# Kernel optimization log

Hardware: AMD Instinct MI355X
Metric: run time of the kernel (lower is better)

The kernel has to match this reference:

```python
import jax, jax.numpy as jnp
import numpy as np

FACTOR = 3.0        # second_match_factor
MAX_DIST = 20.0     # second_match_max_dist
MATCHED_2 = 2       # SPIKE_MATCHED_2
CLID_UNMATCHED = 0

N, S, K = 1_000_000, 64, 32


def setup_inputs() -> dict:
    key = jax.random.key(0)
    k1, k2 = jax.random.split(key)
    return {
        "spikes": jax.random.normal(k1, (N, S), dtype=jnp.float32),
        "sort_idx": jax.random.randint(k2, (N,), 0, K, dtype=jnp.int32),
        "match_idx": jnp.zeros((N,), dtype=jnp.int32),
        "distance": jnp.zeros((N,), dtype=jnp.float32),
        "num_clusters": K,
    }


def reference(spikes, sort_idx, match_idx, distance, num_clusters):
    # spikes: (N, S) float32; sort_idx/match_idx: (N,) int; distance: (N,) float32
    n, s = spikes.shape
    k = int(num_clusters)

    # --- get_means: per-cluster mean waveform and scalar std (sqrt of summed per-dim variance)
    ones = jnp.ones((n,), spikes.dtype)
    counts = jax.ops.segment_sum(ones, sort_idx, num_segments=k)            # (K,)
    sums = jax.ops.segment_sum(spikes, sort_idx, num_segments=k)            # (K, S)
    sumsq = jax.ops.segment_sum(spikes * spikes, sort_idx, num_segments=k)  # (K, S)
    safe = jnp.maximum(counts, 1.0)[:, None]
    means = sums / safe                                                     # (K, S) templates
    var = sumsq / safe - means * means                                      # biased var (np.var ddof=0)
    stds = jnp.sqrt(jnp.maximum(var.sum(axis=1), 0.0))                      # (K,)
    valid = (jnp.arange(k) != CLID_UNMATCHED) & (counts > 0)                # exclude unmatched/empty

    x2 = (spikes * spikes).sum(axis=1, keepdims=True)                       # (N, 1)
    t2 = (means * means).sum(axis=1)                                        # (K,)
    d2 = x2 - 2.0 * (spikes @ means.T) + t2[None, :]
    dist = jnp.sqrt(jnp.maximum(d2, 1e-12))                                 # (N, K)

    # --- threshold mask (> factor*std -> inf) fused with invalid-cluster mask, then argmin
    inf = jnp.asarray(jnp.inf, dist.dtype)
    masked = jnp.where((dist > FACTOR * stds[None, :]) | ~valid[None, :], inf, dist)
    minima = masked.min(axis=1)                                             # (N,)
    minimizers = masked.argmin(axis=1).astype(sort_idx.dtype)               # cluster ids == segment ids
    minimizers = jnp.where(minima >= MAX_DIST * s, CLID_UNMATCHED, minimizers)

    # --- write back only for previously-unmatched spikes (the torch loop covers exactly these)
    unmatched = sort_idx == CLID_UNMATCHED
    new_sort = jnp.where(unmatched, minimizers, sort_idx)
    new_match = jnp.where(unmatched, MATCHED_2, match_idx)
    new_dist = jnp.where(unmatched, minima, distance)
    return new_sort, new_match, new_dist
```

## Files before the change

kernel.cpp:

```cpp
#include <hip/hip_runtime.h>
#include <math.h>

#define SDIM 64
#define KCL  32
#define NPART (KCL*SDIM*2 + KCL)
#define FACTOR_D 3.0
#define MAXDIST_TH 1280.0
#define MATCHED2_F 2.0f

#define SB 1024
#define ST 512
#define BATCH 128

#define ACHUNK 512

__global__ __launch_bounds__(ST) void stats_kernel(
    const float* __restrict__ spikes, const int* __restrict__ sortidx,
    float* __restrict__ pws, int n)
{
  __shared__ float rows[BATCH * SDIM];
  const int lane  = threadIdx.x & 63;
  const int w     = threadIdx.x >> 6;
  const int cbase = w * 4;

  float s0=0,s1=0,s2=0,s3=0;
  float q0=0,q1=0,q2=0,q3=0;
  float cn0=0,cn1=0,cn2=0,cn3=0;

  const long long nbatch = ((long long)n + BATCH - 1) / BATCH;
  const size_t gmax = (size_t)n * SDIM * sizeof(float) - 16;

  float4 v0, v1, v2, v3;
  int ida, idb;

#define LOADBATCH(B)                                                         \
  {                                                                          \
    const long long bsafe = ((B) < nbatch) ? (B) : 0;                        \
    size_t g0 = (size_t)bsafe * BATCH * SDIM * sizeof(float) +               \
                (size_t)threadIdx.x * 16;                                    \
    size_t g1 = g0 + 8192, g2 = g0 + 16384, g3 = g0 + 24576;                 \
    if (g0 > gmax) g0 = gmax;                                                \
    if (g1 > gmax) g1 = gmax;                                                \
    if (g2 > gmax) g2 = gmax;                                                \
    if (g3 > gmax) g3 = gmax;                                                \
    v0 = *reinterpret_cast<const float4*>((const char*)spikes + g0);         \
    v1 = *reinterpret_cast<const float4*>((const char*)spikes + g1);         \
    v2 = *reinterpret_cast<const float4*>((const char*)spikes + g2);         \
    v3 = *reinterpret_cast<const float4*>((const char*)spikes + g3);         \
    const long long ra = bsafe * BATCH + lane, rb = ra + 64;                 \
    ida = ((B) < nbatch && ra < n) ? sortidx[ra] : -1;                       \
    idb = ((B) < nbatch && rb < n) ? sortidx[rb] : -1;                       \
  }

#define POPLOOP(m0,m1,m2,m3,BASE)                                            \
  while (m0 | m1 | m2 | m3) {                                                \
    const bool e0 = m0 != 0, e1 = m1 != 0, e2 = m2 != 0, e3 = m3 != 0;       \
    const int b0 = e0 ? __ffsll(m0) - 1 : 0;                                 \
    const int b1 = e1 ? __ffsll(m1) - 1 : 0;                                 \
    const int b2 = e2 ? __ffsll(m2) - 1 : 0;                                 \
    const int b3 = e3 ? __ffsll(m3) - 1 : 0;                                 \
    m0 &= m0 - 1; m1 &= m1 - 1; m2 &= m2 - 1; m3 &= m3 - 1;                  \
    const float x0 = rows[((BASE) + b0) * SDIM + lane];                      \
    const float x1 = rows[((BASE) + b1) * SDIM + lane];                      \
    const float x2 = rows[((BASE) + b2) * SDIM + lane];                      \
    const float x3 = rows[((BASE) + b3) * SDIM + lane];                      \
    const float y0 = e0 ? x0 : 0.0f, y1 = e1 ? x1 : 0.0f;                    \
    const float y2 = e2 ? x2 : 0.0f, y3 = e3 ? x3 : 0.0f;                    \
    s0 += y0; q0 = fmaf(y0, x0, q0); cn0 += e0 ? 1.0f : 0.0f;                \
    s1 += y1; q1 = fmaf(y1, x1, q1); cn1 += e1 ? 1.0f : 0.0f;                \
    s2 += y2; q2 = fmaf(y2, x2, q2); cn2 += e2 ? 1.0f : 0.0f;                \
    s3 += y3; q3 = fmaf(y3, x3, q3); cn3 += e3 ? 1.0f : 0.0f;                \
  }

  long long bi = blockIdx.x;
  LOADBATCH(bi);

  for (; bi < nbatch; bi += gridDim.x) {
    __syncthreads();
    {
      char* lb = (char*)rows + (size_t)threadIdx.x * 16;
      *reinterpret_cast<float4*>(lb)         = v0;
      *reinterpret_cast<float4*>(lb + 8192)  = v1;
      *reinterpret_cast<float4*>(lb + 16384) = v2;
      *reinterpret_cast<float4*>(lb + 24576) = v3;
    }
    const int cA = ida, cB = idb;
    __syncthreads();

    LOADBATCH(bi + gridDim.x);

    unsigned long long mA0 = __ballot(cA == cbase + 0);
    unsigned long long mA1 = __ballot(cA == cbase + 1);
    unsigned long long mA2 = __ballot(cA == cbase + 2);
    unsigned long long mA3 = __ballot(cA == cbase + 3);
    unsigned long long mB0 = __ballot(cB == cbase + 0);
    unsigned long long mB1 = __ballot(cB == cbase + 1);
    unsigned long long mB2 = __ballot(cB == cbase + 2);
    unsigned long long mB3 = __ballot(cB == cbase + 3);
    if (w == 0) { mA0 = 0; mB0 = 0; }

    POPLOOP(mA0, mA1, mA2, mA3, 0)
    POPLOOP(mB0, mB1, mB2, mB3, 64)
  }
#undef LOADBATCH
#undef POPLOOP

  float* pb = pws + (size_t)blockIdx.x * NPART;
  pb[(cbase + 0) * SDIM + lane] = s0;
  pb[(cbase + 1) * SDIM + lane] = s1;
  pb[(cbase + 2) * SDIM + lane] = s2;
  pb[(cbase + 3) * SDIM + lane] = s3;
  pb[KCL * SDIM + (cbase + 0) * SDIM + lane] = q0;
  pb[KCL * SDIM + (cbase + 1) * SDIM + lane] = q1;
  pb[KCL * SDIM + (cbase + 2) * SDIM + lane] = q2;
  pb[KCL * SDIM + (cbase + 3) * SDIM + lane] = q3;
  if (lane == 0) {
    pb[2 * KCL * SDIM + cbase + 0] = cn0;
    pb[2 * KCL * SDIM + cbase + 1] = cn1;
    pb[2 * KCL * SDIM + cbase + 2] = cn2;
    pb[2 * KCL * SDIM + cbase + 3] = cn3;
  }
}

__global__ __launch_bounds__(1024) void reduce_kernel(
    const float* __restrict__ pws, double* __restrict__ gstats, int nb)
{
  __shared__ double s_acc[16][64];
  const int lane = threadIdx.x & 63;
  const int w    = threadIdx.x >> 6;
  const int u    = blockIdx.x * 64 + lane;
  double acc = 0.0;
  if (u < NPART)
    for (int b = w; b < nb; b += 16)
      acc += (double)pws[(size_t)b * NPART + u];
  s_acc[w][lane] = acc;
  __syncthreads();
  if (w == 0 && u < NPART) {
    double t = 0.0;
#pragma unroll
    for (int j = 0; j < 16; ++j) t += s_acc[j][lane];
    gstats[u] = t;
  }
}

__global__ __launch_bounds__(256) void finalize_kernel(
    const double* __restrict__ gstats, float* __restrict__ means_cs,
    double* __restrict__ t2, double* __restrict__ thr, int* __restrict__ validk)
{
  __shared__ double s_var[KCL], s_t2[KCL];
  if (threadIdx.x < KCL) { s_var[threadIdx.x] = 0.0; s_t2[threadIdx.x] = 0.0; }
  __syncthreads();
  const double* gsum = gstats;
  const double* gsq  = gstats + KCL * SDIM;
  const double* gcnt = gstats + 2 * KCL * SDIM;
  for (int i = threadIdx.x; i < KCL * SDIM; i += blockDim.x) {
    const int c = i / SDIM;
    const double cnt  = gcnt[c];
    const double safe = fmax(cnt, 1.0);
    const double m    = gsum[i] / safe;
    const double var  = gsq[i] / safe - m * m;
    means_cs[i] = (float)m;
    unsafeAtomicAdd(&s_var[c], var);
    unsafeAtomicAdd(&s_t2[c], m * m);
  }
  __syncthreads();
  if (threadIdx.x < KCL) {
    const int c = threadIdx.x;
    thr[c]    = FACTOR_D * sqrt(fmax(s_var[c], 0.0));
    t2[c]     = s_t2[c];
    validk[c] = (c != 0 && gcnt[c] > 0.0) ? 1 : 0;
  }
}

__global__ __launch_bounds__(256) void assign2_kernel(
    const float* __restrict__ spikes, const int* __restrict__ sortidx,
    const int* __restrict__ matchidx, const float* __restrict__ distance,
    const float* __restrict__ means_cs, const double* __restrict__ t2g,
    const double* __restrict__ thrg, const int* __restrict__ validk,
    float* __restrict__ out, int n)
{
  __shared__ float  s_m[KCL][SDIM];
  __shared__ double s_t2[KCL], s_thr[KCL];
  __shared__ int    s_valid[KCL];
  __shared__ int    ids[ACHUNK];
  __shared__ int    scnt;

  for (int i = threadIdx.x; i < KCL * SDIM; i += blockDim.x)
    (&s_m[0][0])[i] = means_cs[i];
  if (threadIdx.x < KCL) {
    s_t2[threadIdx.x]    = t2g[threadIdx.x];
    s_thr[threadIdx.x]   = thrg[threadIdx.x];
    s_valid[threadIdx.x] = validk[threadIdx.x];
  }
  if (threadIdx.x == 0) scnt = 0;
  __syncthreads();

  const long long start = (long long)blockIdx.x * ACHUNK;
  long long end = start + ACHUNK; if (end > n) end = n;

  for (long long i = start + threadIdx.x; i < end; i += blockDim.x) {
    const int cv = sortidx[i];
    if (cv != 0) {
      out[i]           = (float)cv;
      out[n + i]       = (float)matchidx[i];
      out[2LL * n + i] = distance[i];
    } else {
      const int p = atomicAdd(&scnt, 1);
      ids[p] = (int)i;
    }
  }
  __syncthreads();
  const int cnt = scnt;

  for (int base = 0; base < cnt; base += blockDim.x) {
    const int j = base + threadIdx.x;
    if (j >= cnt) break;
    const int r = ids[j];

    float4 xv[16];
    const float4* rp = reinterpret_cast<const float4*>(
        spikes + (size_t)r * SDIM);
#pragma unroll
    for (int s4 = 0; s4 < 16; ++s4) xv[s4] = rp[s4];

    float x2 = 0.0f;
#pragma unroll
    for (int s4 = 0; s4 < 16; ++s4) {
      x2 = fmaf(xv[s4].x, xv[s4].x, x2);
      x2 = fmaf(xv[s4].y, xv[s4].y, x2);
      x2 = fmaf(xv[s4].z, xv[s4].z, x2);
      x2 = fmaf(xv[s4].w, xv[s4].w, x2);
    }

    double best = (double)INFINITY;
    int bidx = 0;
    for (int c = 0; c < KCL; ++c) {
      float dot = 0.0f;
#pragma unroll
      for (int s4 = 0; s4 < 16; ++s4) {
        const float4 m = *reinterpret_cast<const float4*>(&s_m[c][s4 * 4]);
        dot = fmaf(xv[s4].x, m.x, dot);
        dot = fmaf(xv[s4].y, m.y, dot);
        dot = fmaf(xv[s4].z, m.z, dot);
        dot = fmaf(xv[s4].w, m.w, dot);
      }
      if (s_valid[c]) {
        const double d2 = (double)x2 - 2.0 * (double)dot + s_t2[c];
        double dist = sqrt(fmax(d2, 1e-12));
        if (dist <= s_thr[c] && dist < best) { best = dist; bidx = c; }
      }
    }

    const int mz = (best >= MAXDIST_TH) ? 0 : bidx;
    out[r]           = (float)mz;
    out[n + r]       = MATCHED2_F;
    out[2LL * n + r] = (float)best;
  }
}

extern "C" void kernel_launch(void* const* d_in, const int* in_sizes, int n_in,
                              void* d_out, int out_size, void* d_ws, size_t ws_size,
                              hipStream_t stream) {
  const float* spikes   = (const float*)d_in[0];
  const int*   sortidx  = (const int*)d_in[1];
  const int*   matchidx = (const int*)d_in[2];
  const float* distance = (const float*)d_in[3];
  const int n = in_sizes[1];
  if (n <= 0) return;
  float* out = (float*)d_out;

  float*  pws      = (float*)d_ws;
  double* gstats   = (double*)((char*)d_ws +
                               (((size_t)SB * NPART * sizeof(float) + 15) & ~15ull));
  float*  means_cs = (float*)(gstats + NPART);
  double* t2       = (double*)(((size_t)(means_cs + KCL * SDIM) + 7) & ~7ull);
  double* thr      = t2 + KCL;
  int*    validk   = (int*)(thr + KCL);

  const int ablocks = (n + ACHUNK - 1) / ACHUNK;

  stats_kernel<<<SB, ST, 0, stream>>>(spikes, sortidx, pws, n);
  reduce_kernel<<<(NPART + 63) / 64, 1024, 0, stream>>>(pws, gstats, SB);
  finalize_kernel<<<1, 256, 0, stream>>>(gstats, means_cs, t2, thr, validk);
  assign2_kernel<<<ablocks, 256, 0, stream>>>(spikes, sortidx, matchidx,
                                              distance, means_cs, t2, thr,
                                              validk, out, n);
}
```

Before: 109.9 us.

## Drop LDS staging in stats kernel; read spike rows directly per wave

The stats kernel no longer stages 128-row batches in shared memory behind block barriers. Each block now owns a contiguous chunk of rows, and every wave scans the sort indices 64 rows at a time, using ballots to load only rows of its own clusters straight from global memory (256B coalesced per row). Counts now come from popcount instead of per-iteration increments. This removes the barriers and the LDS traffic, but every row is fetched by a single wave through dependent global loads inside the pop loop, so latency may be exposed and there is no register prefetch of row data.

```diff
diff --git a/kernel.cpp b/kernel.cpp
--- a/kernel.cpp
+++ b/kernel.cpp
@@ -10,15 +10,13 @@
 
 #define SB 1024
 #define ST 512
-#define BATCH 128
 
 #define ACHUNK 512
 
 __global__ __launch_bounds__(ST) void stats_kernel(
     const float* __restrict__ spikes, const int* __restrict__ sortidx,
-    float* __restrict__ pws, int n)
-{
-  __shared__ float rows[BATCH * SDIM];
+    float* __restrict__ pws, int n, int chunk)
+{
   const int lane  = threadIdx.x & 63;
   const int w     = threadIdx.x >> 6;
   const int cbase = w * 4;
@@ -27,83 +25,49 @@
   float q0=0,q1=0,q2=0,q3=0;
   float cn0=0,cn1=0,cn2=0,cn3=0;
 
-  const long long nbatch = ((long long)n + BATCH - 1) / BATCH;
-  const size_t gmax = (size_t)n * SDIM * sizeof(float) - 16;
-
-  float4 v0, v1, v2, v3;
-  int ida, idb;
-
-#define LOADBATCH(B)                                                         \
-  {                                                                          \
-    const long long bsafe = ((B) < nbatch) ? (B) : 0;                        \
-    size_t g0 = (size_t)bsafe * BATCH * SDIM * sizeof(float) +               \
-                (size_t)threadIdx.x * 16;                                    \
-    size_t g1 = g0 + 8192, g2 = g0 + 16384, g3 = g0 + 24576;                 \
-    if (g0 > gmax) g0 = gmax;                                                \
-    if (g1 > gmax) g1 = gmax;                                                \
-    if (g2 > gmax) g2 = gmax;                                                \
-    if (g3 > gmax) g3 = gmax;                                                \
-    v0 = *reinterpret_cast<const float4*>((const char*)spikes + g0);         \
-    v1 = *reinterpret_cast<const float4*>((const char*)spikes + g1);         \
-    v2 = *reinterpret_cast<const float4*>((const char*)spikes + g2);         \
-    v3 = *reinterpret_cast<const float4*>((const char*)spikes + g3);         \
-    const long long ra = bsafe * BATCH + lane, rb = ra + 64;                 \
-    ida = ((B) < nbatch && ra < n) ? sortidx[ra] : -1;                       \
-    idb = ((B) < nbatch && rb < n) ? sortidx[rb] : -1;                       \
-  }
-
-#define POPLOOP(m0,m1,m2,m3,BASE)                                            \
-  while (m0 | m1 | m2 | m3) {                                                \
-    const bool e0 = m0 != 0, e1 = m1 != 0, e2 = m2 != 0, e3 = m3 != 0;       \
-    const int b0 = e0 ? __ffsll(m0) - 1 : 0;                                 \
-    const int b1 = e1 ? __ffsll(m1) - 1 : 0;                                 \
-    const int b2 = e2 ? __ffsll(m2) - 1 : 0;                                 \
-    const int b3 = e3 ? __ffsll(m3) - 1 : 0;                                 \
-    m0 &= m0 - 1; m1 &= m1 - 1; m2 &= m2 - 1; m3 &= m3 - 1;                  \
-    const float x0 = rows[((BASE) + b0) * SDIM + lane];                      \
-    const float x1 = rows[((BASE) + b1) * SDIM + lane];                      \
-    const float x2 = rows[((BASE) + b2) * SDIM + lane];                      \
-    const float x3 = rows[((BASE) + b3) * SDIM + lane];                      \
-    const float y0 = e0 ? x0 : 0.0f, y1 = e1 ? x1 : 0.0f;                    \
-    const float y2 = e2 ? x2 : 0.0f, y3 = e3 ? x3 : 0.0f;                    \
-    s0 += y0; q0 = fmaf(y0, x0, q0); cn0 += e0 ? 1.0f : 0.0f;                \
-    s1 += y1; q1 = fmaf(y1, x1, q1); cn1 += e1 ? 1.0f : 0.0f;                \
-    s2 += y2; q2 = fmaf(y2, x2, q2); cn2 += e2 ? 1.0f : 0.0f;                \
-    s3 += y3; q3 = fmaf(y3, x3, q3); cn3 += e3 ? 1.0f : 0.0f;                \
-  }
-
-  long long bi = blockIdx.x;
-  LOADBATCH(bi);
-
-  for (; bi < nbatch; bi += gridDim.x) {
-    __syncthreads();
-    {
-      char* lb = (char*)rows + (size_t)threadIdx.x * 16;
-      *reinterpret_cast<float4*>(lb)         = v0;
-      *reinterpret_cast<float4*>(lb + 8192)  = v1;
-      *reinterpret_cast<float4*>(lb + 16384) = v2;
-      *reinterpret_cast<float4*>(lb + 24576) = v3;
-    }
-    const int cA = ida, cB = idb;
-    __syncthreads();
-
-    LOADBATCH(bi + gridDim.x);
-
-    unsigned long long mA0 = __ballot(cA == cbase + 0);
-    unsigned long long mA1 = __ballot(cA == cbase + 1);
-    unsigned long long mA2 = __ballot(cA == cbase + 2);
-    unsigned long long mA3 = __ballot(cA == cbase + 3);
-    unsigned long long mB0 = __ballot(cB == cbase + 0);
-    unsigned long long mB1 = __ballot(cB == cbase + 1);
-    unsigned long long mB2 = __ballot(cB == cbase + 2);
-    unsigned long long mB3 = __ballot(cB == cbase + 3);
-    if (w == 0) { mA0 = 0; mB0 = 0; }
-
-    POPLOOP(mA0, mA1, mA2, mA3, 0)
-    POPLOOP(mB0, mB1, mB2, mB3, 64)
-  }
-#undef LOADBATCH
-#undef POPLOOP
+  const long long start = (long long)blockIdx.x * chunk;
+  long long end = start + chunk; if (end > n) end = n;
+
+  if (start < end) {
+    long long il = start + lane;
+    int id_cur = (il < end) ? sortidx[il] : -1;
+
+    for (long long wb = start; wb < end; wb += 64) {
+      const long long nl = wb + 64 + lane;
+      const int id_next = (nl < end) ? sortidx[nl] : -1;
+
+      unsigned long long m0 = __ballot(id_cur == cbase + 0);
+      unsigned long long m1 = __ballot(id_cur == cbase + 1);
+      unsigned long long m2 = __ballot(id_cur == cbase + 2);
+      unsigned long long m3 = __ballot(id_cur == cbase + 3);
+      if (w == 0) m0 = 0;
+
+      cn0 += (float)__popcll(m0);
+      cn1 += (float)__popcll(m1);
+      cn2 += (float)__popcll(m2);
+      cn3 += (float)__popcll(m3);
+
+      while (m0 | m1 | m2 | m3) {
+        const bool e0 = m0 != 0, e1 = m1 != 0, e2 = m2 != 0, e3 = m3 != 0;
+        const int b0 = e0 ? __ffsll(m0) - 1 : 0;
+        const int b1 = e1 ? __ffsll(m1) - 1 : 0;
+        const int b2 = e2 ? __ffsll(m2) - 1 : 0;
+        const int b3 = e3 ? __ffsll(m3) - 1 : 0;
+        m0 &= m0 - 1; m1 &= m1 - 1; m2 &= m2 - 1; m3 &= m3 - 1;
+        const float x0 = spikes[(size_t)(wb + b0) * SDIM + lane];
+        const float x1 = spikes[(size_t)(wb + b1) * SDIM + lane];
+        const float x2 = spikes[(size_t)(wb + b2) * SDIM + lane];
+        const float x3 = spikes[(size_t)(wb + b3) * SDIM + lane];
+        const float y0 = e0 ? x0 : 0.0f, y1 = e1 ? x1 : 0.0f;
+        const float y2 = e2 ? x2 : 0.0f, y3 = e3 ? x3 : 0.0f;
+        s0 += y0; q0 = fmaf(y0, x0, q0);
+        s1 += y1; q1 = fmaf(y1, x1, q1);
+        s2 += y2; q2 = fmaf(y2, x2, q2);
+        s3 += y3; q3 = fmaf(y3, x3, q3);
+      }
+      id_cur = id_next;
+    }
+  }
 
   float* pb = pws + (size_t)blockIdx.x * NPART;
   pb[(cbase + 0) * SDIM + lane] = s0;
@@ -277,9 +241,10 @@
   double* thr      = t2 + KCL;
   int*    validk   = (int*)(thr + KCL);
 
+  const int chunk   = (int)((((long long)n + SB - 1) / SB + 63) & ~63LL);
   const int ablocks = (n + ACHUNK - 1) / ACHUNK;
 
-  stats_kernel<<<SB, ST, 0, stream>>>(spikes, sortidx, pws, n);
+  stats_kernel<<<SB, ST, 0, stream>>>(spikes, sortidx, pws, n, chunk);
   reduce_kernel<<<(NPART + 63) / 64, 1024, 0, stream>>>(pws, gstats, SB);
   finalize_kernel<<<1, 256, 0, stream>>>(gstats, means_cs, t2, thr, validk);
   assign2_kernel<<<ablocks, 256, 0, stream>>>(spikes, sortidx, matchidx,
```

Measured after the change: 129.1 us. +17.5%, slower.

## Process four spike rows per wave step using float4 sub-groups in stats kernel

Applied to the files above, without the earlier changes.

The per-cluster accumulation loop is restructured so each wave splits into four 16-lane groups. Each group reads a different matching row as a float4, so one wave processes up to four rows of the same cluster per iteration instead of one row each for four clusters in lockstep. Counts come from popcount, and partial sums are combined with cross-lane shuffles before vectorized stores. This cuts loop iterations and LDS read instructions, at the cost of extra selection logic per iteration and a final shuffle reduction.

```diff
diff --git a/kernel.cpp b/kernel.cpp
--- a/kernel.cpp
+++ b/kernel.cpp
@@ -19,13 +19,15 @@
     float* __restrict__ pws, int n)
 {
   __shared__ float rows[BATCH * SDIM];
-  const int lane  = threadIdx.x & 63;
-  const int w     = threadIdx.x >> 6;
+  const int lane = threadIdx.x & 63;
+  const int w    = threadIdx.x >> 6;
   const int cbase = w * 4;
-
-  float s0=0,s1=0,s2=0,s3=0;
-  float q0=0,q1=0,q2=0,q3=0;
-  float cn0=0,cn1=0,cn2=0,cn3=0;
+  const int g    = lane >> 4;
+  const int l    = lane & 15;
+
+  float4 s0 = make_float4(0,0,0,0), s1 = s0, s2 = s0, s3 = s0;
+  float4 q0 = s0, q1 = s0, q2 = s0, q3 = s0;
+  float cn0 = 0, cn1 = 0, cn2 = 0, cn3 = 0;
 
   const long long nbatch = ((long long)n + BATCH - 1) / BATCH;
   const size_t gmax = (size_t)n * SDIM * sizeof(float) - 16;
@@ -52,24 +54,43 @@
     idb = ((B) < nbatch && rb < n) ? sortidx[rb] : -1;                       \
   }
 
-#define POPLOOP(m0,m1,m2,m3,BASE)                                            \
-  while (m0 | m1 | m2 | m3) {                                                \
-    const bool e0 = m0 != 0, e1 = m1 != 0, e2 = m2 != 0, e3 = m3 != 0;       \
-    const int b0 = e0 ? __ffsll(m0) - 1 : 0;                                 \
-    const int b1 = e1 ? __ffsll(m1) - 1 : 0;                                 \
-    const int b2 = e2 ? __ffsll(m2) - 1 : 0;                                 \
-    const int b3 = e3 ? __ffsll(m3) - 1 : 0;                                 \
-    m0 &= m0 - 1; m1 &= m1 - 1; m2 &= m2 - 1; m3 &= m3 - 1;                  \
-    const float x0 = rows[((BASE) + b0) * SDIM + lane];                      \
-    const float x1 = rows[((BASE) + b1) * SDIM + lane];                      \
-    const float x2 = rows[((BASE) + b2) * SDIM + lane];                      \
-    const float x3 = rows[((BASE) + b3) * SDIM + lane];                      \
-    const float y0 = e0 ? x0 : 0.0f, y1 = e1 ? x1 : 0.0f;                    \
-    const float y2 = e2 ? x2 : 0.0f, y3 = e3 ? x3 : 0.0f;                    \
-    s0 += y0; q0 = fmaf(y0, x0, q0); cn0 += e0 ? 1.0f : 0.0f;                \
-    s1 += y1; q1 = fmaf(y1, x1, q1); cn1 += e1 ? 1.0f : 0.0f;                \
-    s2 += y2; q2 = fmaf(y2, x2, q2); cn2 += e2 ? 1.0f : 0.0f;                \
-    s3 += y3; q3 = fmaf(y3, x3, q3); cn3 += e3 ? 1.0f : 0.0f;                \
+#define DOCLUSTER(SJ, QJ, CNJ, MA, MB)                                       \
+  {                                                                          \
+    unsigned long long a = (MA), b = (MB);                                   \
+    CNJ += (float)(__popcll(a) + __popcll(b));                               \
+    while (a | b) {                                                          \
+      const int nA = __popcll(a);                                            \
+      const int total = nA + __popcll(b);                                    \
+      const bool useB = g >= nA;                                             \
+      const unsigned long long mm = useB ? b : a;                            \
+      const int want = useB ? (g - nA) : g;                                  \
+      const unsigned long long u1 = mm & (mm - 1);                           \
+      const unsigned long long u2 = u1 & (u1 - 1);                           \
+      const unsigned long long u3 = u2 & (u2 - 1);                           \
+      const unsigned long long sel =                                         \
+          (want == 0) ? mm : (want == 1) ? u1 : (want == 2) ? u2 : u3;       \
+      const bool valid = (g < total) && (sel != 0ull);                       \
+      const int bit = __ffsll(sel) - 1;                                      \
+      const int rowi = valid ? ((useB ? 64 : 0) + bit) : 0;                  \
+      const float4 x = *reinterpret_cast<const float4*>(                     \
+          &rows[rowi * SDIM + l * 4]);                                       \
+      const float4 y = valid ? x : make_float4(0.f, 0.f, 0.f, 0.f);          \
+      SJ.x += y.x; QJ.x = fmaf(y.x, x.x, QJ.x);                              \
+      SJ.y += y.y; QJ.y = fmaf(y.y, x.y, QJ.y);                              \
+      SJ.z += y.z; QJ.z = fmaf(y.z, x.z, QJ.z);                              \
+      SJ.w += y.w; QJ.w = fmaf(y.w, x.w, QJ.w);                              \
+      const int take = total < 4 ? total : 4;                                \
+      const int tA = take < nA ? take : nA;                                  \
+      const int tB = take - tA;                                              \
+      if (tA > 0) a &= a - 1;                                                \
+      if (tA > 1) a &= a - 1;                                                \
+      if (tA > 2) a &= a - 1;                                                \
+      if (tA > 3) a &= a - 1;                                                \
+      if (tB > 0) b &= b - 1;                                                \
+      if (tB > 1) b &= b - 1;                                                \
+      if (tB > 2) b &= b - 1;                                                \
+      if (tB > 3) b &= b - 1;                                                \
+    }                                                                        \
   }
 
   long long bi = blockIdx.x;
@@ -90,30 +111,44 @@
     LOADBATCH(bi + gridDim.x);
 
     unsigned long long mA0 = __ballot(cA == cbase + 0);
-    unsigned long long mA1 = __ballot(cA == cbase + 1);
-    unsigned long long mA2 = __ballot(cA == cbase + 2);
-    unsigned long long mA3 = __ballot(cA == cbase + 3);
     unsigned long long mB0 = __ballot(cB == cbase + 0);
-    unsigned long long mB1 = __ballot(cB == cbase + 1);
-    unsigned long long mB2 = __ballot(cB == cbase + 2);
-    unsigned long long mB3 = __ballot(cB == cbase + 3);
     if (w == 0) { mA0 = 0; mB0 = 0; }
-
-    POPLOOP(mA0, mA1, mA2, mA3, 0)
-    POPLOOP(mB0, mB1, mB2, mB3, 64)
+    const unsigned long long mA1 = __ballot(cA == cbase + 1);
+    const unsigned long long mB1 = __ballot(cB == cbase + 1);
+    const unsigned long long mA2 = __ballot(cA == cbase + 2);
+    const unsigned long long mB2 = __ballot(cB == cbase + 2);
+    const unsigned long long mA3 = __ballot(cA == cbase + 3);
+    const unsigned long long mB3 = __ballot(cB == cbase + 3);
+
+    DOCLUSTER(s0, q0, cn0, mA0, mB0)
+    DOCLUSTER(s1, q1, cn1, mA1, mB1)
+    DOCLUSTER(s2, q2, cn2, mA2, mB2)
+    DOCLUSTER(s3, q3, cn3, mA3, mB3)
   }
 #undef LOADBATCH
-#undef POPLOOP
+#undef DOCLUSTER
+
+#define XRED(V)                                                              \
+  V.x += __shfl_xor(V.x, 32, 64); V.y += __shfl_xor(V.y, 32, 64);            \
+  V.z += __shfl_xor(V.z, 32, 64); V.w += __shfl_xor(V.w, 32, 64);            \
+  V.x += __shfl_xor(V.x, 16, 64); V.y += __shfl_xor(V.y, 16, 64);            \
+  V.z += __shfl_xor(V.z, 16, 64); V.w += __shfl_xor(V.w, 16, 64);
+  XRED(s0) XRED(s1) XRED(s2) XRED(s3)
+  XRED(q0) XRED(q1) XRED(q2) XRED(q3)
+#undef XRED
 
   float* pb = pws + (size_t)blockIdx.x * NPART;
-  pb[(cbase + 0) * SDIM + lane] = s0;
-  pb[(cbase + 1) * SDIM + lane] = s1;
-  pb[(cbase + 2) * SDIM + lane] = s2;
-  pb[(cbase + 3) * SDIM + lane] = s3;
-  pb[KCL * SDIM + (cbase + 0) * SDIM + lane] = q0;
-  pb[KCL * SDIM + (cbase + 1) * SDIM + lane] = q1;
-  pb[KCL * SDIM + (cbase + 2) * SDIM + lane] = q2;
-  pb[KCL * SDIM + (cbase + 3) * SDIM + lane] = q3;
+  if (g == 0) {
+    *reinterpret_cast<float4*>(&pb[(cbase + 0) * SDIM + l * 4]) = s0;
+    *reinterpret_cast<float4*>(&pb[(cbase + 1) * SDIM + l * 4]) = s1;
+    *reinterpret_cast<float4*>(&pb[(cbase + 2) * SDIM + l * 4]) = s2;
+    *reinterpret_cast<float4*>(&pb[(cbase + 3) * SDIM + l * 4]) = s3;
+    float* pq = pb + KCL * SDIM;
+    *reinterpret_cast<float4*>(&pq[(cbase + 0) * SDIM + l * 4]) = q0;
+    *reinterpret_cast<float4*>(&pq[(cbase + 1) * SDIM + l * 4]) = q1;
+    *reinterpret_cast<float4*>(&pq[(cbase + 2) * SDIM + l * 4]) = q2;
+    *reinterpret_cast<float4*>(&pq[(cbase + 3) * SDIM + l * 4]) = q3;
+  }
   if (lane == 0) {
     pb[2 * KCL * SDIM + cbase + 0] = cn0;
     pb[2 * KCL * SDIM + cbase + 1] = cn1;
```

Result: slower. 133.1 us (+21.1%).

## Stage stats rows via direct global-to-LDS loads and fuse reduce with finalize

Applied to the files above, without the earlier changes.

The stats kernel now double-buffers rows in LDS and fills them with global_load_lds, so the next batch streams in while the current one is accumulated, with no register staging. The grid is halved to 512 blocks. The reduce and finalize kernels are merged into one launch, where a last-block ticket (reset by the stats kernel) runs the finalize step, removing a kernel launch. The cost is double the LDS per block, which can lower occupancy. The ticket pattern also relies on correct fences and kernel ordering.

```diff
diff --git a/kernel.cpp b/kernel.cpp
--- a/kernel.cpp
+++ b/kernel.cpp
@@ -8,17 +8,20 @@
 #define MAXDIST_TH 1280.0
 #define MATCHED2_F 2.0f
 
-#define SB 1024
+#define SB 512
 #define ST 512
 #define BATCH 128
 
 #define ACHUNK 512
+#define RBLK 65
 
 __global__ __launch_bounds__(ST) void stats_kernel(
     const float* __restrict__ spikes, const int* __restrict__ sortidx,
-    float* __restrict__ pws, int n)
+    float* __restrict__ pws, int* __restrict__ ticket, int n)
 {
-  __shared__ float rows[BATCH * SDIM];
+  __shared__ float rows[2][BATCH * SDIM];
+  if (blockIdx.x == 0 && threadIdx.x == 0) *ticket = 0;
+
   const int lane  = threadIdx.x & 63;
   const int w     = threadIdx.x >> 6;
   const int cbase = w * 4;
@@ -30,29 +33,32 @@
   const long long nbatch = ((long long)n + BATCH - 1) / BATCH;
   const size_t gmax = (size_t)n * SDIM * sizeof(float) - 16;
 
-  float4 v0, v1, v2, v3;
   int ida, idb;
-
-#define LOADBATCH(B)                                                         \
+  int ina, inb;
+
+#define STAGE(B, BUF)                                                        \
   {                                                                          \
-    const long long bsafe = ((B) < nbatch) ? (B) : 0;                        \
-    size_t g0 = (size_t)bsafe * BATCH * SDIM * sizeof(float) +               \
-                (size_t)threadIdx.x * 16;                                    \
-    size_t g1 = g0 + 8192, g2 = g0 + 16384, g3 = g0 + 24576;                 \
-    if (g0 > gmax) g0 = gmax;                                                \
-    if (g1 > gmax) g1 = gmax;                                                \
-    if (g2 > gmax) g2 = gmax;                                                \
-    if (g3 > gmax) g3 = gmax;                                                \
-    v0 = *reinterpret_cast<const float4*>((const char*)spikes + g0);         \
-    v1 = *reinterpret_cast<const float4*>((const char*)spikes + g1);         \
-    v2 = *reinterpret_cast<const float4*>((const char*)spikes + g2);         \
-    v3 = *reinterpret_cast<const float4*>((const char*)spikes + g3);         \
-    const long long ra = bsafe * BATCH + lane, rb = ra + 64;                 \
-    ida = ((B) < nbatch && ra < n) ? sortidx[ra] : -1;                       \
-    idb = ((B) < nbatch && rb < n) ? sortidx[rb] : -1;                       \
-  }
-
-#define POPLOOP(m0,m1,m2,m3,BASE)                                            \
+    const size_t gb = (size_t)(B) * BATCH * SDIM * sizeof(float);            \
+    _Pragma("unroll")                                                        \
+    for (int k = 0; k < 4; ++k) {                                            \
+      size_t go = gb + (size_t)k * 8192 + (size_t)threadIdx.x * 16;          \
+      if (go > gmax) go = gmax;                                              \
+      const float* gp = (const float*)((const char*)spikes + go);            \
+      float* lp = &rows[BUF][(k * 8192 + w * 1024) >> 2];                    \
+      __builtin_amdgcn_global_load_lds(                                      \
+          (const __attribute__((address_space(1))) float*)gp,                \
+          (__attribute__((address_space(3))) float*)lp, 16, 0, 0);           \
+    }                                                                        \
+  }
+
+#define LOADIDS(B, RA, RB)                                                   \
+  {                                                                          \
+    const long long r0 = (long long)(B) * BATCH + lane;                      \
+    RA = (r0 < n) ? sortidx[r0] : -1;                                        \
+    RB = (r0 + 64 < n) ? sortidx[r0 + 64] : -1;                              \
+  }
+
+#define POPLOOP(m0,m1,m2,m3,BASE,RC)                                         \
   while (m0 | m1 | m2 | m3) {                                                \
     const bool e0 = m0 != 0, e1 = m1 != 0, e2 = m2 != 0, e3 = m3 != 0;       \
     const int b0 = e0 ? __ffsll(m0) - 1 : 0;                                 \
@@ -60,10 +66,10 @@
     const int b2 = e2 ? __ffsll(m2) - 1 : 0;                                 \
     const int b3 = e3 ? __ffsll(m3) - 1 : 0;                                 \
     m0 &= m0 - 1; m1 &= m1 - 1; m2 &= m2 - 1; m3 &= m3 - 1;                  \
-    const float x0 = rows[((BASE) + b0) * SDIM + lane];                      \
-    const float x1 = rows[((BASE) + b1) * SDIM + lane];                      \
-    const float x2 = rows[((BASE) + b2) * SDIM + lane];                      \
-    const float x3 = rows[((BASE) + b3) * SDIM + lane];                      \
+    const float x0 = RC[((BASE) + b0) * SDIM + lane];                        \
+    const float x1 = RC[((BASE) + b1) * SDIM + lane];                        \
+    const float x2 = RC[((BASE) + b2) * SDIM + lane];                        \
+    const float x3 = RC[((BASE) + b3) * SDIM + lane];                        \
     const float y0 = e0 ? x0 : 0.0f, y1 = e1 ? x1 : 0.0f;                    \
     const float y2 = e2 ? x2 : 0.0f, y3 = e3 ? x3 : 0.0f;                    \
     s0 += y0; q0 = fmaf(y0, x0, q0); cn0 += e0 ? 1.0f : 0.0f;                \
@@ -73,36 +79,39 @@
   }
 
   long long bi = blockIdx.x;
-  LOADBATCH(bi);
+  int cur = 0;
+  if (bi < nbatch) {
+    STAGE(bi, 0)
+    LOADIDS(bi, ida, idb)
+  }
+  __syncthreads();
 
   for (; bi < nbatch; bi += gridDim.x) {
+    const long long bn = bi + gridDim.x;
+    if (bn < nbatch) {
+      STAGE(bn, cur ^ 1)
+      LOADIDS(bn, ina, inb)
+    }
+
+    unsigned long long mA0 = __ballot(ida == cbase + 0);
+    unsigned long long mA1 = __ballot(ida == cbase + 1);
+    unsigned long long mA2 = __ballot(ida == cbase + 2);
+    unsigned long long mA3 = __ballot(ida == cbase + 3);
+    unsigned long long mB0 = __ballot(idb == cbase + 0);
+    unsigned long long mB1 = __ballot(idb == cbase + 1);
+    unsigned long long mB2 = __ballot(idb == cbase + 2);
+    unsigned long long mB3 = __ballot(idb == cbase + 3);
+    if (w == 0) { mA0 = 0; mB0 = 0; }
+
+    const float* rc = rows[cur];
+    POPLOOP(mA0, mA1, mA2, mA3, 0,  rc)
+    POPLOOP(mB0, mB1, mB2, mB3, 64, rc)
+
     __syncthreads();
-    {
-      char* lb = (char*)rows + (size_t)threadIdx.x * 16;
-      *reinterpret_cast<float4*>(lb)         = v0;
-      *reinterpret_cast<float4*>(lb + 8192)  = v1;
-      *reinterpret_cast<float4*>(lb + 16384) = v2;
-      *reinterpret_cast<float4*>(lb + 24576) = v3;
-    }
-    const int cA = ida, cB = idb;
-    __syncthreads();
-
-    LOADBATCH(bi + gridDim.x);
-
-    unsigned long long mA0 = __ballot(cA == cbase + 0);
-    unsigned long long mA1 = __ballot(cA == cbase + 1);
-    unsigned long long mA2 = __ballot(cA == cbase + 2);
-    unsigned long long mA3 = __ballot(cA == cbase + 3);
-    unsigned long long mB0 = __ballot(cB == cbase + 0);
-    unsigned long long mB1 = __ballot(cB == cbase + 1);
-    unsigned long long mB2 = __ballot(cB == cbase + 2);
-    unsigned long long mB3 = __ballot(cB == cbase + 3);
-    if (w == 0) { mA0 = 0; mB0 = 0; }
-
-    POPLOOP(mA0, mA1, mA2, mA3, 0)
-    POPLOOP(mB0, mB1, mB2, mB3, 64)
-  }
-#undef LOADBATCH
+    cur ^= 1; ida = ina; idb = inb;
+  }
+#undef STAGE
+#undef LOADIDS
 #undef POPLOOP
 
   float* pb = pws + (size_t)blockIdx.x * NPART;
@@ -122,31 +131,39 @@
   }
 }
 
-__global__ __launch_bounds__(1024) void reduce_kernel(
-    const float* __restrict__ pws, double* __restrict__ gstats, int nb)
+__global__ __launch_bounds__(1024) void reduce_finalize_kernel(
+    const float* __restrict__ pws, double* __restrict__ gstats,
+    float* __restrict__ means_cs, double* __restrict__ t2,
+    double* __restrict__ thr, int* __restrict__ validk,
+    int* __restrict__ ticket, int nb)
 {
-  __shared__ double s_acc[16][64];
-  const int lane = threadIdx.x & 63;
-  const int w    = threadIdx.x >> 6;
-  const int u    = blockIdx.x * 64 + lane;
-  double acc = 0.0;
-  if (u < NPART)
-    for (int b = w; b < nb; b += 16)
-      acc += (double)pws[(size_t)b * NPART + u];
-  s_acc[w][lane] = acc;
-  __syncthreads();
-  if (w == 0 && u < NPART) {
-    double t = 0.0;
+  {
+    __shared__ double s_acc[16][64];
+    const int lane = threadIdx.x & 63;
+    const int w    = threadIdx.x >> 6;
+    const int u    = blockIdx.x * 64 + lane;
+    double acc = 0.0;
+    if (u < NPART)
+      for (int b = w; b < nb; b += 16)
+        acc += (double)pws[(size_t)b * NPART + u];
+    s_acc[w][lane] = acc;
+    __syncthreads();
+    if (w == 0 && u < NPART) {
+      double t = 0.0;
 #pragma unroll
-    for (int j = 0; j < 16; ++j) t += s_acc[j][lane];
-    gstats[u] = t;
-  }
-}
-
-__global__ __launch_bounds__(256) void finalize_kernel(
-    const double* __restrict__ gstats, float* __restrict__ means_cs,
-    double* __restrict__ t2, double* __restrict__ thr, int* __restrict__ validk)
-{
+      for (int j = 0; j < 16; ++j) t += s_acc[j][lane];
+      gstats[u] = t;
+    }
+  }
+
+  __threadfence();
+  __shared__ int isLast;
+  if (threadIdx.x == 0)
+    isLast = (atomicAdd(ticket, 1) == (int)gridDim.x - 1) ? 1 : 0;
+  __syncthreads();
+  if (!isLast) return;
+  __threadfence();
+
   __shared__ double s_var[KCL], s_t2[KCL];
   if (threadIdx.x < KCL) { s_var[threadIdx.x] = 0.0; s_t2[threadIdx.x] = 0.0; }
   __syncthreads();
@@ -276,12 +293,13 @@
   double* t2       = (double*)(((size_t)(means_cs + KCL * SDIM) + 7) & ~7ull);
   double* thr      = t2 + KCL;
   int*    validk   = (int*)(thr + KCL);
+  int*    ticket   = validk + KCL;
 
   const int ablocks = (n + ACHUNK - 1) / ACHUNK;
 
-  stats_kernel<<<SB, ST, 0, stream>>>(spikes, sortidx, pws, n);
-  reduce_kernel<<<(NPART + 63) / 64, 1024, 0, stream>>>(pws, gstats, SB);
-  finalize_kernel<<<1, 256, 0, stream>>>(gstats, means_cs, t2, thr, validk);
+  stats_kernel<<<SB, ST, 0, stream>>>(spikes, sortidx, pws, ticket, n);
+  reduce_finalize_kernel<<<RBLK, 1024, 0, stream>>>(pws, gstats, means_cs,
+                                                    t2, thr, validk, ticket, SB);
   assign2_kernel<<<ablocks, 256, 0, stream>>>(spikes, sortidx, matchidx,
                                               distance, means_cs, t2, thr,
                                               validk, out, n);
```

Result: slower. 123.7 us (+12.5%).
